# Kernel tuning notes

Hardware: AMD Instinct MI355X
Metric: run time of the kernel (lower is better)

Reference implementation:

```python
import jax, jax.numpy as jnp
import numpy as np

NUM_VOXEL_X = 128
NUM_VOXEL_Y = 128
NUM_CHANNELS = 80


def setup_inputs() -> dict:
    key = jax.random.key(0)
    k1, k2, k3 = jax.random.split(key, 3)
    B, N, D, H, W = 2, 6, 112, 16, 44
    total = B * N * D * H * W
    geom_xyz = jax.random.randint(k1, (total, 3), 0, 128, dtype=jnp.int64 if jax.config.jax_enable_x64 else jnp.int32).astype(jnp.int32)
    depth_features = jax.random.uniform(k2, (total,), dtype=jnp.float32)
    context_features = jax.random.normal(k3, (B, N, NUM_CHANNELS, H, W), dtype=jnp.float32)
    return {
        "geom_xyz": geom_xyz,
        "depth_features": depth_features,
        "context_features": context_features,
        "batch_size": B,
        "num_cams": N,
        "num_depth": D,
        "num_height": H,
        "num_width": W,
    }


def reference(geom_xyz, depth_features, context_features, batch_size, num_cams, num_depth, num_height, num_width):
    B, N, D, H, W = batch_size, num_cams, num_depth, num_height, num_width
    C = NUM_CHANNELS
    total = B * N * D * H * W

    # per-point feature = depth * context (context does not depend on depth bin)
    depth = depth_features.reshape(B, N, D, H, W)
    ctx = jnp.transpose(context_features, (0, 1, 3, 4, 2))  # (B,N,H,W,C)
    feats = depth[..., None] * ctx[:, :, None, :, :, :]      # (B,N,D,H,W,C)
    feats = feats.reshape(total, C)

    x = geom_xyz[:, 0].astype(jnp.int32)
    y = geom_xyz[:, 1].astype(jnp.int32)
    valid = (x >= 0) & (x < NUM_VOXEL_X) & (y >= 0) & (y < NUM_VOXEL_Y)

    batch_idx = (jnp.arange(total, dtype=jnp.int32) // (N * D * H * W))
    flat_idx = batch_idx * (NUM_VOXEL_Y * NUM_VOXEL_X) + jnp.clip(y, 0, NUM_VOXEL_Y - 1) * NUM_VOXEL_X + jnp.clip(x, 0, NUM_VOXEL_X - 1)

    feats = jnp.where(valid[:, None], feats, 0.0)
    out = jax.ops.segment_sum(feats, flat_idx, num_segments=B * NUM_VOXEL_Y * NUM_VOXEL_X)
    return out.reshape(B, NUM_VOXEL_Y, NUM_VOXEL_X, C)
```

## Files before the change

### kernel.cpp

```cpp
#include <hip/hip_runtime.h>


namespace {
constexpr int NVX = 128, NVY = 128, C = 80;
constexpr int B = 2, N = 6, D = 112, H = 16, W = 44;
constexpr int HW    = H * W;
constexpr int BN    = B * N;
constexpr int DHW   = D * HW;
constexpr int NDHW  = N * DHW;
constexpr int TOTAL = B * NDHW;
constexpr int NVOX  = B * NVY * NVX;

constexpr int NBIN  = 512;
constexpr int VPB   = NVOX / NBIN;
constexpr int SLOT  = 8;
constexpr int CAP   = 7;
constexpr int PTS_PER_BLK = 1024;
constexpr int SCAN_BLOCKS = TOTAL / PTS_PER_BLK;
constexpr int TR_BLOCKS   = BN * (C / 16) * (HW / 64);
constexpr int PRE_BLOCKS  = SCAN_BLOCKS + TR_BLOCKS;
constexpr int SPILLCAP = 65536;

constexpr int VCAP = 57;
constexpr int OCAP = 32;
}

__global__ __launch_bounds__(256) void pre_kernel(
    const int*   __restrict__ geom, const float* __restrict__ depth,
    const float* __restrict__ ctx,  float* __restrict__ ctx_t,
    int2* __restrict__ staging, int* __restrict__ spillcnt,
    int2* __restrict__ spill)
{
    __shared__ int2  stage[NBIN * SLOT];
    __shared__ int   bcnt[NBIN];
    __shared__ float tile[16 * 68];

    const int t = threadIdx.x;
    if (blockIdx.x < SCAN_BLOCKS) {
        const int lane = t & 63;
        bcnt[t] = 0; bcnt[t + 256] = 0;
        __syncthreads();

        const int p0 = blockIdx.x * PTS_PER_BLK + t * 4;
        const int4* g4 = (const int4*)(geom + (size_t)3 * p0);
        const int4 q0 = g4[0], q1 = g4[1], q2 = g4[2];
        const float4 dp = *(const float4*)(depth + p0);
        const int xs[4] = {q0.x, q0.w, q1.z, q2.y};
        const int ys[4] = {q0.y, q1.x, q1.w, q2.z};
        const int db[4] = {__float_as_int(dp.x), __float_as_int(dp.y),
                           __float_as_int(dp.z), __float_as_int(dp.w)};

        int bnv = (int)((unsigned)p0 / (unsigned)DHW);
        int rem = p0 - bnv * DHW;
        int hwv = rem % HW;
        const int bb = (blockIdx.x >= SCAN_BLOCKS / 2) ? 1 : 0;

        int bins[4], keys[4], idxv[4];
        #pragma unroll
        for (int u = 0; u < 4; ++u) {
            const int x = xs[u], y = ys[u];
            const bool ok = (unsigned)x < (unsigned)NVX &&
                            (unsigned)y < (unsigned)NVY;
            const int v   = (bb * NVY + y) * NVX + x;
            const int row = bnv * HW + hwv;
            bins[u] = v & 511;
            keys[u] = (v << 14) | row;
            idxv[u] = ok ? -1 : -2;
            ++rem; ++hwv;
            if (rem == DHW)      { rem = 0; ++bnv; hwv = 0; }
            else if (hwv == HW)  { hwv = 0; }
        }
        #pragma unroll
        for (int u = 0; u < 4; ++u)
            if (idxv[u] == -1) idxv[u] = atomicAdd(&bcnt[bins[u]], 1);
        #pragma unroll
        for (int u = 0; u < 4; ++u)
            if ((unsigned)idxv[u] < (unsigned)CAP)
                stage[bins[u] * SLOT + idxv[u]] = make_int2(keys[u], db[u]);
        #pragma unroll
        for (int u = 0; u < 4; ++u) {
            const bool sp = (idxv[u] >= CAP);
            const unsigned long long m = __ballot(sp);
            if (m) {
                const int leader = (int)__ffsll((unsigned long long)m) - 1;
                int base = 0;
                if (lane == leader) base = atomicAdd(spillcnt, (int)__popcll(m));
                base = __shfl(base, leader);
                if (sp) {
                    const int off = base +
                        (int)__popcll(m & ((1ull << lane) - 1ull));
                    if (off < SPILLCAP) spill[off] = make_int2(keys[u], db[u]);
                }
            }
        }
        __syncthreads();
        stage[t * SLOT + CAP].x = bcnt[t];
        stage[(t + 256) * SLOT + CAP].x = bcnt[t + 256];
        __syncthreads();

        const int4* src = (const int4*)stage;
        int4* dst = (int4*)staging;
        #pragma unroll
        for (int k = 0; k < 8; ++k) {
            const int i  = k * 256 + t;
            const int sl = i >> 2, part = i & 3;
            dst[((size_t)sl * SCAN_BLOCKS + blockIdx.x) * 4 + part] = src[i];
        }
    } else {
        const int tb  = blockIdx.x - SCAN_BLOCKS;
        const int bn  = tb / 55;
        const int rem = tb % 55;
        const int c0  = (rem / 11) * 16;
        const int hw0 = (rem % 11) * 64;
        const int cl = t >> 6, hwl = t & 63;
        #pragma unroll
        for (int r = 0; r < 4; ++r) {
            const int c = r * 4 + cl;
            tile[c * 68 + hwl] =
                ctx[(size_t)(bn * C + c0 + c) * HW + hw0 + hwl];
        }
        __syncthreads();
        const int cr = t & 15, hwr = t >> 4;
        #pragma unroll
        for (int r = 0; r < 4; ++r) {
            const int hw = r * 16 + hwr;
            ctx_t[(size_t)(bn * HW + hw0 + hw) * C + c0 + cr] =
                tile[cr * 68 + hw];
        }
    }
}

__global__ __launch_bounds__(1024) void acc_kernel(
    const int2* __restrict__ staging, const float* __restrict__ ctx_t,
    float* __restrict__ out, const int* __restrict__ spillcnt,
    const int2* __restrict__ spill)
{
    __shared__ int2 list[VPB * VCAP];
    __shared__ int  vcnt[VPB];
    __shared__ int  ocnt;
    __shared__ int2 olist[OCAP];

    const int bin  = blockIdx.x;
    const int t    = threadIdx.x;
    const int wave = t >> 6, lane = t & 63;

    if (t < VPB) vcnt[t] = 0;
    if (t == 0) ocnt = 0;
    __syncthreads();

    const int g8 = lane >> 3, slot = lane & 7;
    constexpr int NCH = (SCAN_BLOCKS + 7) / 8;
    {
        auto ldchunk = [&](int c) -> int2 {
            const int s = c * 8 + g8;
            return (c < NCH && s < SCAN_BLOCKS)
                ? staging[((size_t)bin * SCAN_BLOCKS + s) * SLOT + slot]
                : make_int2(0, 0);
        };
        int2 eA = ldchunk(wave);
        int2 eB = ldchunk(wave + 16);
        for (int c = wave; c < NCH; c += 16) {
            const int2 e = eA;
            eA = eB;
            eB = ldchunk(c + 32);
            const int s = c * 8 + g8;
            int cnt = __shfl(e.x, (lane & 56) | CAP);
            cnt = cnt < CAP ? cnt : CAP;
            if (s < SCAN_BLOCKS && slot < cnt) {
                const int vl  = e.x >> 23;
                const int idx = atomicAdd(&vcnt[vl], 1);
                if (idx < VCAP) list[vl * VCAP + idx] = e;
                else { int o = atomicAdd(&ocnt, 1); if (o < OCAP) olist[o] = e; }
            }
        }
    }
    {
        int scnt = *spillcnt;
        scnt = scnt < SPILLCAP ? scnt : SPILLCAP;
        for (int i = t; i < scnt; i += 1024) {
            const int2 e = spill[i];
            if (((e.x >> 14) & 511) == bin) {
                const int vl  = e.x >> 23;
                const int idx = atomicAdd(&vcnt[vl], 1);
                if (idx < VCAP) list[vl * VCAP + idx] = e;
                else { int o = atomicAdd(&ocnt, 1); if (o < OCAP) olist[o] = e; }
            }
        }
    }
    __syncthreads();

    const int g3 = lane / 20;
    const int p  = lane % 20;
    const int ch0 = p * 4;
    for (int vv = 0; vv < VPB / 16; ++vv) {
        const int vl = wave * (VPB / 16) + vv;
        int n = vcnt[vl];
        n = n < VCAP ? n : VCAP;
        const int2* lp = list + vl * VCAP;

        float4 s = make_float4(0.f, 0.f, 0.f, 0.f);
        for (int j = 0; j < n; j += 12) {
            #pragma unroll
            for (int k = 0; k < 4; ++k) {
                const int idx = j + k * 3 + g3;
                const bool ok = (g3 < 3) && (idx < n);
                const int2 e = lp[ok ? idx : 0];
                const float w = ok ? __int_as_float(e.y) : 0.f;
                const int row = e.x & 16383;
                const float4 cf =
                    *(const float4*)(ctx_t + (size_t)row * C + ch0);
                s.x += w * cf.x; s.y += w * cf.y;
                s.z += w * cf.z; s.w += w * cf.w;
            }
        }
        float4 r;
        r.x = s.x + __shfl(s.x, p + 20) + __shfl(s.x, p + 40);
        r.y = s.y + __shfl(s.y, p + 20) + __shfl(s.y, p + 40);
        r.z = s.z + __shfl(s.z, p + 20) + __shfl(s.z, p + 40);
        r.w = s.w + __shfl(s.w, p + 20) + __shfl(s.w, p + 40);
        if (lane < 20) {
            float* o = out + (size_t)((vl << 9) | bin) * C;
            *(float4*)(o + ch0) = r;
        }
    }
    __syncthreads();

    if (wave == 0) {
        int oc = ocnt;
        oc = oc < OCAP ? oc : OCAP;
        for (int i = 0; i < oc; ++i) {
            const int2 e = olist[i];
            const int vl = e.x >> 23, row = e.x & 16383;
            const float dep = __int_as_float(e.y);
            const float* c = ctx_t + (size_t)row * C;
            float* o = out + (size_t)((vl << 9) | bin) * C;
            unsafeAtomicAdd(o + lane, dep * c[lane]);
            if (lane < 16) unsafeAtomicAdd(o + 64 + lane, dep * c[64 + lane]);
        }
    }
}

extern "C" void kernel_launch(void* const* d_in, const int* in_sizes, int n_in,
                              void* d_out, int out_size, void* d_ws, size_t ws_size,
                              hipStream_t stream) {
    const int*   geom  = (const int*)d_in[0];
    const float* depth = (const float*)d_in[1];
    const float* ctx   = (const float*)d_in[2];
    float*       out   = (float*)d_out;

    char* ws = (char*)d_ws;
    int2* staging  = (int2*)ws; ws += (size_t)NBIN * SCAN_BLOCKS * SLOT * 8;
    int2* spill    = (int2*)ws; ws += (size_t)SPILLCAP * 8;
    int*  spillcnt = (int*)ws;  ws += 256;
    float* ctx_t   = (float*)ws;

    hipMemsetAsync(spillcnt, 0, 256, stream);

    pre_kernel<<<dim3(PRE_BLOCKS), dim3(256),  0, stream>>>(
                  geom, depth, ctx, ctx_t, staging, spillcnt, spill);
    acc_kernel<<<dim3(NBIN),       dim3(1024), 0, stream>>>(
                  staging, ctx_t, out, spillcnt, spill);
}
```

Baseline: 109.0 us.

## Replace fixed-slot bin staging with per-block counting sort and prefix offsets

Each scan block now counting-sorts its 1024 points by bin into a dense shared array, using a block-wide prefix scan, and writes that array plus per-bin start/end offsets. The accumulation kernel reads only the offsets and entries for its own bin, instead of scanning padded 8-slot records and a global spill list. This removes the spill atomics, the memset and the padded staging traffic, which shrinks the workspace. The cost is an extra prefix scan per scan block. Each thread in acc_kernel also walks a variable-length range serially, and the loads from the dense per-block arrays are uncoalesced. Invalid points are mapped to bin 0 with zero weight, so bin 0 carries extra work.

```diff
diff --git a/kernel.cpp b/kernel.cpp
--- a/kernel.cpp
+++ b/kernel.cpp
@@ -13,13 +13,10 @@
 
 constexpr int NBIN  = 512;
 constexpr int VPB   = NVOX / NBIN;
-constexpr int SLOT  = 8;
-constexpr int CAP   = 7;
 constexpr int PTS_PER_BLK = 1024;
 constexpr int SCAN_BLOCKS = TOTAL / PTS_PER_BLK;
 constexpr int TR_BLOCKS   = BN * (C / 16) * (HW / 64);
 constexpr int PRE_BLOCKS  = SCAN_BLOCKS + TR_BLOCKS;
-constexpr int SPILLCAP = 65536;
 
 constexpr int VCAP = 57;
 constexpr int OCAP = 32;
@@ -28,16 +25,16 @@
 __global__ __launch_bounds__(256) void pre_kernel(
     const int*   __restrict__ geom, const float* __restrict__ depth,
     const float* __restrict__ ctx,  float* __restrict__ ctx_t,
-    int2* __restrict__ staging, int* __restrict__ spillcnt,
-    int2* __restrict__ spill)
+    int2* __restrict__ staging, uint2* __restrict__ pfxbuf)
 {
-    __shared__ int2  stage[NBIN * SLOT];
     __shared__ int   bcnt[NBIN];
+    __shared__ unsigned short pfxl[NBIN];
+    __shared__ int2  dense[PTS_PER_BLK];
+    __shared__ int   wsum[4];
     __shared__ float tile[16 * 68];
 
     const int t = threadIdx.x;
     if (blockIdx.x < SCAN_BLOCKS) {
-        const int lane = t & 63;
         bcnt[t] = 0; bcnt[t + 256] = 0;
         __syncthreads();
 
@@ -47,15 +44,15 @@
         const float4 dp = *(const float4*)(depth + p0);
         const int xs[4] = {q0.x, q0.w, q1.z, q2.y};
         const int ys[4] = {q0.y, q1.x, q1.w, q2.z};
-        const int db[4] = {__float_as_int(dp.x), __float_as_int(dp.y),
-                           __float_as_int(dp.z), __float_as_int(dp.w)};
+        const int dbi[4] = {__float_as_int(dp.x), __float_as_int(dp.y),
+                            __float_as_int(dp.z), __float_as_int(dp.w)};
 
         int bnv = (int)((unsigned)p0 / (unsigned)DHW);
         int rem = p0 - bnv * DHW;
         int hwv = rem % HW;
         const int bb = (blockIdx.x >= SCAN_BLOCKS / 2) ? 1 : 0;
 
-        int bins[4], keys[4], idxv[4];
+        int bins[4], keys[4], wts[4], idxv[4];
         #pragma unroll
         for (int u = 0; u < 4; ++u) {
             const int x = xs[u], y = ys[u];
@@ -63,49 +60,49 @@
                             (unsigned)y < (unsigned)NVY;
             const int v   = (bb * NVY + y) * NVX + x;
             const int row = bnv * HW + hwv;
-            bins[u] = v & 511;
-            keys[u] = (v << 14) | row;
-            idxv[u] = ok ? -1 : -2;
+            bins[u] = ok ? (v & 511) : 0;
+            keys[u] = ok ? ((v << 14) | row) : 0;
+            wts[u]  = ok ? dbi[u] : 0;
             ++rem; ++hwv;
-            if (rem == DHW)      { rem = 0; ++bnv; hwv = 0; }
-            else if (hwv == HW)  { hwv = 0; }
+            if (rem == DHW)     { rem = 0; ++bnv; hwv = 0; }
+            else if (hwv == HW) { hwv = 0; }
         }
         #pragma unroll
         for (int u = 0; u < 4; ++u)
-            if (idxv[u] == -1) idxv[u] = atomicAdd(&bcnt[bins[u]], 1);
+            idxv[u] = atomicAdd(&bcnt[bins[u]], 1);
+        __syncthreads();
+
+        const int lane = t & 63, wv = t >> 6;
+        const int c0 = bcnt[2 * t], c1 = bcnt[2 * t + 1];
+        const int pair = c0 + c1;
+        int incl = pair;
+        #pragma unroll
+        for (int off = 1; off < 64; off <<= 1) {
+            const int nb = __shfl_up(incl, off);
+            if (lane >= off) incl += nb;
+        }
+        if (lane == 63) wsum[wv] = incl;
+        __syncthreads();
+        int woff = 0;
+        if (wv > 0) woff += wsum[0];
+        if (wv > 1) woff += wsum[1];
+        if (wv > 2) woff += wsum[2];
+        const int ex = woff + incl - pair;
+        pfxl[2 * t]     = (unsigned short)ex;
+        pfxl[2 * t + 1] = (unsigned short)(ex + c0);
+        pfxbuf[(size_t)blockIdx.x * 256 + t] = make_uint2(
+            ((unsigned)ex << 16)        | (unsigned)(ex + c0),
+            ((unsigned)(ex + c0) << 16) | (unsigned)(ex + pair));
+        __syncthreads();
+
         #pragma unroll
         for (int u = 0; u < 4; ++u)
-            if ((unsigned)idxv[u] < (unsigned)CAP)
-                stage[bins[u] * SLOT + idxv[u]] = make_int2(keys[u], db[u]);
-        #pragma unroll
-        for (int u = 0; u < 4; ++u) {
-            const bool sp = (idxv[u] >= CAP);
-            const unsigned long long m = __ballot(sp);
-            if (m) {
-                const int leader = (int)__ffsll((unsigned long long)m) - 1;
-                int base = 0;
-                if (lane == leader) base = atomicAdd(spillcnt, (int)__popcll(m));
-                base = __shfl(base, leader);
-                if (sp) {
-                    const int off = base +
-                        (int)__popcll(m & ((1ull << lane) - 1ull));
-                    if (off < SPILLCAP) spill[off] = make_int2(keys[u], db[u]);
-                }
-            }
-        }
-        __syncthreads();
-        stage[t * SLOT + CAP].x = bcnt[t];
-        stage[(t + 256) * SLOT + CAP].x = bcnt[t + 256];
-        __syncthreads();
-
-        const int4* src = (const int4*)stage;
-        int4* dst = (int4*)staging;
-        #pragma unroll
-        for (int k = 0; k < 8; ++k) {
-            const int i  = k * 256 + t;
-            const int sl = i >> 2, part = i & 3;
-            dst[((size_t)sl * SCAN_BLOCKS + blockIdx.x) * 4 + part] = src[i];
-        }
+            dense[(int)pfxl[bins[u]] + idxv[u]] = make_int2(keys[u], wts[u]);
+        __syncthreads();
+        const int4* src = (const int4*)dense;
+        int4* dst = (int4*)staging + (size_t)blockIdx.x * 512;
+        dst[t]       = src[t];
+        dst[t + 256] = src[t + 256];
     } else {
         const int tb  = blockIdx.x - SCAN_BLOCKS;
         const int bn  = tb / 55;
@@ -131,9 +128,8 @@
 }
 
 __global__ __launch_bounds__(1024) void acc_kernel(
-    const int2* __restrict__ staging, const float* __restrict__ ctx_t,
-    float* __restrict__ out, const int* __restrict__ spillcnt,
-    const int2* __restrict__ spill)
+    const int2* __restrict__ staging, const unsigned* __restrict__ pfx32,
+    const float* __restrict__ ctx_t, float* __restrict__ out)
 {
     __shared__ int2 list[VPB * VCAP];
     __shared__ int  vcnt[VPB];
@@ -148,43 +144,15 @@
     if (t == 0) ocnt = 0;
     __syncthreads();
 
-    const int g8 = lane >> 3, slot = lane & 7;
-    constexpr int NCH = (SCAN_BLOCKS + 7) / 8;
-    {
-        auto ldchunk = [&](int c) -> int2 {
-            const int s = c * 8 + g8;
-            return (c < NCH && s < SCAN_BLOCKS)
-                ? staging[((size_t)bin * SCAN_BLOCKS + s) * SLOT + slot]
-                : make_int2(0, 0);
-        };
-        int2 eA = ldchunk(wave);
-        int2 eB = ldchunk(wave + 16);
-        for (int c = wave; c < NCH; c += 16) {
-            const int2 e = eA;
-            eA = eB;
-            eB = ldchunk(c + 32);
-            const int s = c * 8 + g8;
-            int cnt = __shfl(e.x, (lane & 56) | CAP);
-            cnt = cnt < CAP ? cnt : CAP;
-            if (s < SCAN_BLOCKS && slot < cnt) {
-                const int vl  = e.x >> 23;
-                const int idx = atomicAdd(&vcnt[vl], 1);
-                if (idx < VCAP) list[vl * VCAP + idx] = e;
-                else { int o = atomicAdd(&ocnt, 1); if (o < OCAP) olist[o] = e; }
-            }
-        }
-    }
-    {
-        int scnt = *spillcnt;
-        scnt = scnt < SPILLCAP ? scnt : SPILLCAP;
-        for (int i = t; i < scnt; i += 1024) {
-            const int2 e = spill[i];
-            if (((e.x >> 14) & 511) == bin) {
-                const int vl  = e.x >> 23;
-                const int idx = atomicAdd(&vcnt[vl], 1);
-                if (idx < VCAP) list[vl * VCAP + idx] = e;
-                else { int o = atomicAdd(&ocnt, 1); if (o < OCAP) olist[o] = e; }
-            }
+    for (int sb = t; sb < SCAN_BLOCKS; sb += 1024) {
+        const unsigned se = pfx32[(size_t)sb * NBIN + bin];
+        const int s = (int)(se >> 16), e = (int)(se & 0xFFFFu);
+        for (int i = s; i < e; ++i) {
+            const int2 en = staging[(size_t)sb * PTS_PER_BLK + i];
+            const int vl  = en.x >> 23;
+            const int idx = atomicAdd(&vcnt[vl], 1);
+            if (idx < VCAP) list[vl * VCAP + idx] = en;
+            else { int o = atomicAdd(&ocnt, 1); if (o < OCAP) olist[o] = en; }
         }
     }
     __syncthreads();
@@ -249,15 +217,12 @@
     float*       out   = (float*)d_out;
 
     char* ws = (char*)d_ws;
-    int2* staging  = (int2*)ws; ws += (size_t)NBIN * SCAN_BLOCKS * SLOT * 8;
-    int2* spill    = (int2*)ws; ws += (size_t)SPILLCAP * 8;
-    int*  spillcnt = (int*)ws;  ws += 256;
+    int2*  staging = (int2*)ws;  ws += (size_t)SCAN_BLOCKS * PTS_PER_BLK * 8;
+    uint2* pfxbuf  = (uint2*)ws; ws += (size_t)SCAN_BLOCKS * NBIN * 4;
     float* ctx_t   = (float*)ws;
 
-    hipMemsetAsync(spillcnt, 0, 256, stream);
-
     pre_kernel<<<dim3(PRE_BLOCKS), dim3(256),  0, stream>>>(
-                  geom, depth, ctx, ctx_t, staging, spillcnt, spill);
+                  geom, depth, ctx, ctx_t, staging, pfxbuf);
     acc_kernel<<<dim3(NBIN),       dim3(1024), 0, stream>>>(
-                  staging, ctx_t, out, spillcnt, spill);
-}
+                  staging, (const unsigned*)pfxbuf, ctx_t, out);
+}
```

Result: no change. 110.2 us (+1.1%).
